# Optimization experiments

Hardware: AMD Instinct MI355X
Metric: run time of the kernel (lower is better)

The kernel has to match this reference:

```python
import jax, jax.numpy as jnp
import numpy as np

N = 200000   # total nodes across batched graphs
E = 3200000  # total edges
G = 1024     # number of graphs
MOL_DIM, HID, OUT = 9, 64, 64


def gcn_conv(x, W, b, src, dst, num_nodes):
    """PyG GCNConv: add self-loops, symmetric deg^{-1/2} normalization, linear first."""
    x = x @ W  # [N, H]
    loop = jnp.arange(num_nodes, dtype=src.dtype)
    s = jnp.concatenate([src, loop])
    d = jnp.concatenate([dst, loop])
    deg = jax.ops.segment_sum(jnp.ones_like(d, dtype=x.dtype), d, num_segments=num_nodes)
    dinv = jnp.where(deg > 0, jax.lax.rsqrt(deg), 0.0)
    norm = dinv[s] * dinv[d]                       # [E+N]
    msgs = x[s] * norm[:, None]                    # gather + scale
    out = jax.ops.segment_sum(msgs, d, num_segments=num_nodes)  # scatter-add
    return out + b


def setup_inputs() -> dict:
    key = jax.random.key(0)
    ks = jax.random.split(key, 12)
    def glorot(k, shp):
        scale = np.sqrt(2.0 / (shp[0] + shp[1])).astype(np.float32)
        return jax.random.normal(k, shp, dtype=jnp.float32) * scale
    return {
        "x": jax.random.normal(ks[0], (N, MOL_DIM), dtype=jnp.float32),
        "edge_index": jax.random.randint(ks[1], (2, E), 0, N, dtype=jnp.int32),
        "edge_attr": jax.random.normal(ks[2], (E, 3), dtype=jnp.float32),
        "batch": jnp.sort(jax.random.randint(ks[3], (N,), 0, G, dtype=jnp.int32)),
        "W1": glorot(ks[4], (MOL_DIM, HID)), "b1": jnp.zeros((HID,), jnp.float32),
        "W2": glorot(ks[5], (HID, HID)),     "b2": jnp.zeros((HID,), jnp.float32),
        "W3": glorot(ks[6], (HID, HID)),     "b3": jnp.zeros((HID,), jnp.float32),
        "Wl": glorot(ks[7], (2 * HID, OUT)), "bl": jnp.zeros((OUT,), jnp.float32),
    }


def reference(x, edge_index, edge_attr, batch, W1, b1, W2, b2, W3, b3, Wl, bl):
    src, dst = edge_index[0], edge_index[1]
    h = jax.nn.relu(gcn_conv(x, W1, b1, src, dst, N))
    h = jax.nn.relu(gcn_conv(h, W2, b2, src, dst, N))
    h = jax.nn.relu(gcn_conv(h, W3, b3, src, dst, N))
    # global mean/max pool over graphs
    counts = jax.ops.segment_sum(jnp.ones((N,), h.dtype), batch, num_segments=G)
    h_sum = jax.ops.segment_sum(h, batch, num_segments=G)
    h_mean = h_sum / jnp.maximum(counts, 1.0)[:, None]
    h_max = jax.ops.segment_max(h, batch, num_segments=G)
    pooled = jnp.concatenate([h_mean, h_max], axis=1)   # [G, 2H]
    return pooled @ Wl + bl
```

## Files before the change

kernel.cpp:

```cpp
#include <hip/hip_runtime.h>

typedef unsigned short u16;
typedef __attribute__((ext_vector_type(8))) short short8;
typedef __attribute__((ext_vector_type(4))) float float4v;

#define HID 64
#define MOLD 9
#define BSH 10
#define NBM 256
#define NBLK 256

__device__ __forceinline__ float bf2f(u16 u) {
    return __uint_as_float(((unsigned)u) << 16);
}
__device__ __forceinline__ u16 f2bf(float f) {
    unsigned x = __float_as_uint(f);
    unsigned r = (x + 0x7FFFu + ((x >> 16) & 1u)) >> 16;
    return (u16)r;
}
__device__ __forceinline__ void unpack_add(uint4 r, float* a) {
    a[0] += __uint_as_float(r.x << 16); a[1] += __uint_as_float(r.x & 0xffff0000u);
    a[2] += __uint_as_float(r.y << 16); a[3] += __uint_as_float(r.y & 0xffff0000u);
    a[4] += __uint_as_float(r.z << 16); a[5] += __uint_as_float(r.z & 0xffff0000u);
    a[6] += __uint_as_float(r.w << 16); a[7] += __uint_as_float(r.w & 0xffff0000u);
}
__device__ __forceinline__ void unpack_set(uint4 r, float* a) {
    a[0] = __uint_as_float(r.x << 16); a[1] = __uint_as_float(r.x & 0xffff0000u);
    a[2] = __uint_as_float(r.y << 16); a[3] = __uint_as_float(r.y & 0xffff0000u);
    a[4] = __uint_as_float(r.z << 16); a[5] = __uint_as_float(r.z & 0xffff0000u);
    a[6] = __uint_as_float(r.w << 16); a[7] = __uint_as_float(r.w & 0xffff0000u);
}

__global__ void k_detect(const u16* __restrict__ p, int n, int* __restrict__ flag) {
    bool bad = false;
    for (int i = threadIdx.x; i < n; i += 256) {
        float v = bf2f(p[i]);
        if (!(v == v) || fabsf(v) > 1000.f) bad = true;
    }
    if (bad) atomicOr(flag, 1);
}

__device__ __forceinline__ void cvt_seg(const void* src, u16* dst, int n, int mode) {
    if (mode) {
        const float* s = (const float*)src;
        for (int i = threadIdx.x; i < n; i += 256) dst[i] = f2bf(s[i]);
    } else {
        const u16* s = (const u16*)src;
        for (int i = threadIdx.x; i < n; i += 256) dst[i] = s[i];
    }
}

__global__ void k_cvt_w(const void* W1, const void* b1, const void* W2, const void* b2,
                        const void* W3, const void* b3, const void* Wl, const void* bl,
                        const int* __restrict__ flag, u16* __restrict__ wbf) {
    int mode = *flag;
    cvt_seg(W1, wbf + 0,     MOLD * HID, mode);
    cvt_seg(b1, wbf + 576,   HID, mode);
    cvt_seg(W2, wbf + 640,   HID * HID, mode);
    cvt_seg(b2, wbf + 4736,  HID, mode);
    cvt_seg(W3, wbf + 4800,  HID * HID, mode);
    cvt_seg(b3, wbf + 8896,  HID, mode);
    cvt_seg(Wl, wbf + 8960,  2 * HID * HID, mode);
    cvt_seg(bl, wbf + 17152, HID, mode);
}

__global__ void k_cvt_x(const void* __restrict__ src, u16* __restrict__ dst, int n,
                        const int* __restrict__ flag) {
    int mode = *flag;
    int i = blockIdx.x * 256 + threadIdx.x;
    if (i >= n) return;
    dst[i] = mode ? f2bf(((const float*)src)[i]) : ((const u16*)src)[i];
}

__global__ __launch_bounds__(256) void k_hist(const int* __restrict__ ei, int E, int nb,
                                              int chunk, int* __restrict__ cntmat) {
    __shared__ int h[NBM];
    int tid = threadIdx.x, k = blockIdx.x;
    for (int i = tid; i < nb; i += 256) h[i] = 0;
    __syncthreads();
    int e0 = k * chunk, e1 = e0 + chunk; if (e1 > E) e1 = E;
    for (int e = e0 + tid; e < e1; e += 256)
        atomicAdd(&h[ei[E + e] >> BSH], 1);
    __syncthreads();
    for (int b = tid; b < nb; b += 256) cntmat[b * NBLK + k] = h[b];
}

__global__ __launch_bounds__(1024) void k_scanmat(int* __restrict__ cntmat, int total) {
    __shared__ int ps[1024];
    int tid = threadIdx.x;
    int chunk = (total + 1023) >> 10;
    int i0 = tid * chunk, i1 = i0 + chunk; if (i1 > total) i1 = total;
    int sum = 0;
    for (int i = i0; i < i1; i++) sum += cntmat[i];
    ps[tid] = sum;
    __syncthreads();
    for (int off = 1; off < 1024; off <<= 1) {
        int t = (tid >= off) ? ps[tid - off] : 0;
        __syncthreads();
        ps[tid] += t;
        __syncthreads();
    }
    int run = ps[tid] - sum;
    for (int i = i0; i < i1; i++) { int c = cntmat[i]; cntmat[i] = run; run += c; }
}

__global__ __launch_bounds__(256) void k_scatter(const int* __restrict__ ei, int E, int nb,
                                                 int chunk, const int* __restrict__ offmat,
                                                 unsigned* __restrict__ staging) {
    __shared__ int cur[NBM];
    int tid = threadIdx.x, k = blockIdx.x;
    for (int b = tid; b < nb; b += 256) cur[b] = offmat[b * NBLK + k];
    __syncthreads();
    int e0 = k * chunk, e1 = e0 + chunk; if (e1 > E) e1 = E;
    for (int e = e0 + tid; e < e1; e += 256) {
        int s = ei[e];
        int d = ei[E + e];
        int b = d >> BSH;
        int p = atomicAdd(&cur[b], 1);
        staging[p] = (unsigned)s | ((unsigned)(d & ((1 << BSH) - 1)) << 18);
    }
}

__global__ __launch_bounds__(256) void k_p4(const unsigned* __restrict__ staging,
                                            const int* __restrict__ offmat, int nb, int N, int E,
                                            int* __restrict__ col, int* __restrict__ rowptr,
                                            float* __restrict__ dinv) {
    __shared__ int cnt[1 << BSH];
    __shared__ int cur[1 << BSH];
    __shared__ int ps[256];
    int b = blockIdx.x, tid = threadIdx.x;
    int s0 = offmat[b * NBLK];
    int s1 = (b == nb - 1) ? E : offmat[(b + 1) * NBLK];
    for (int i = tid; i < (1 << BSH); i += 256) cnt[i] = 0;
    __syncthreads();
    for (int i = s0 + tid; i < s1; i += 256)
        atomicAdd(&cnt[staging[i] >> 18], 1);
    __syncthreads();
    int base4 = tid * 4;
    int c0 = cnt[base4], c1 = cnt[base4 + 1], c2 = cnt[base4 + 2], c3 = cnt[base4 + 3];
    int tsum = c0 + c1 + c2 + c3;
    ps[tid] = tsum;
    __syncthreads();
    for (int off = 1; off < 256; off <<= 1) {
        int t = (tid >= off) ? ps[tid - off] : 0;
        __syncthreads();
        ps[tid] += t;
        __syncthreads();
    }
    int ex = ps[tid] - tsum;
    int o0 = s0 + ex, o1 = o0 + c0, o2 = o1 + c1, o3 = o2 + c2;
    cur[base4] = o0; cur[base4 + 1] = o1; cur[base4 + 2] = o2; cur[base4 + 3] = o3;
    int v = (b << BSH) + base4;
    if (v < N)     { rowptr[v] = o0;     dinv[v] = rsqrtf((float)(c0 + 1)); }
    if (v + 1 < N) { rowptr[v + 1] = o1; dinv[v + 1] = rsqrtf((float)(c1 + 1)); }
    if (v + 2 < N) { rowptr[v + 2] = o2; dinv[v + 2] = rsqrtf((float)(c2 + 1)); }
    if (v + 3 < N) { rowptr[v + 3] = o3; dinv[v + 3] = rsqrtf((float)(c3 + 1)); }
    if (b == nb - 1 && tid == 0) rowptr[N] = E;
    __syncthreads();
    for (int i = s0 + tid; i < s1; i += 256) {
        unsigned w = staging[i];
        int p = atomicAdd(&cur[w >> 18], 1);
        col[p] = (int)(w & 0x3FFFF);
    }
}

__global__ void k_l1(const u16* __restrict__ x, const u16* __restrict__ wseg,
                     const float* __restrict__ dinv, int N, u16* __restrict__ y) {
    __shared__ float w[MOLD * HID];
    int tid = threadIdx.x;
    for (int i = tid; i < MOLD * HID; i += blockDim.x) w[i] = bf2f(wseg[i]);
    __syncthreads();
    int v = blockIdx.x * 4 + (tid >> 6);
    int f = tid & 63;
    if (v >= N) return;
    float acc = 0.f;
#pragma unroll
    for (int k = 0; k < MOLD; k++) acc += bf2f(x[v * MOLD + k]) * w[k * HID + f];
    y[v * HID + f] = f2bf(dinv[v] * acc);
}

__device__ __forceinline__ float gather_node_one(const u16* __restrict__ y,
                                                 const int* __restrict__ rowptr,
                                                 const int* __restrict__ col,
                                                 float dv, float bias,
                                                 int v, int eslot, int fg) {
    float acc[8];
    const u16* yf = y + fg * 8;
    if (eslot == 0) {
        unpack_set(*(const uint4*)(yf + (size_t)v * HID), acc);
    } else {
#pragma unroll
        for (int j = 0; j < 8; j++) acc[j] = 0.f;
    }
    int e = rowptr[v + 1];
    for (int i = rowptr[v] + eslot; i < e; i += 8) {
        int u = col[i];
        uint4 r = *(const uint4*)(yf + (size_t)u * HID);
        unpack_add(r, acc);
    }
    bool e0 = (eslot & 1) != 0, e1 = (eslot & 2) != 0, e2 = (eslot & 4) != 0;
    float s[8];
#pragma unroll
    for (int j = 0; j < 8; j++) s[j] = acc[j] + __shfl_xor(acc[j], 8);
    float b4[4];
#pragma unroll
    for (int k = 0; k < 4; k++) b4[k] = e0 ? s[k + 4] : s[k];
#pragma unroll
    for (int k = 0; k < 4; k++) b4[k] += __shfl_xor(b4[k], 16);
    float c2[2];
    c2[0] = e1 ? b4[2] : b4[0];
    c2[1] = e1 ? b4[3] : b4[1];
    c2[0] += __shfl_xor(c2[0], 32);
    c2[1] += __shfl_xor(c2[1], 32);
    float val = e2 ? c2[1] : c2[0];
    return fmaxf(dv * val + bias, 0.f);
}

__global__ __launch_bounds__(256, 4) void k_agg(
        const u16* __restrict__ y, const int* __restrict__ rowptr,
        const int* __restrict__ col, const float* __restrict__ dinv,
        const u16* __restrict__ bseg, int N, u16* __restrict__ h) {
    int lane = threadIdx.x & 63;
    int eslot = lane >> 3, fg = lane & 7;
    int idx = fg * 8 + ((eslot & 1) << 2) + (eslot & 2) + ((eslot >> 2) & 1);
    float bias = bf2f(bseg[idx]);
    int wid = (blockIdx.x * blockDim.x + threadIdx.x) >> 6;
    int nw = (gridDim.x * blockDim.x) >> 6;
    for (int v = wid; v < N; v += nw) {
        float hv = gather_node_one(y, rowptr, col, dinv[v], bias, v, eslot, fg);
        h[(size_t)v * HID + idx] = f2bf(hv);
    }
}

__global__ __launch_bounds__(256, 4) void k_aggpool(
        const u16* __restrict__ y, const int* __restrict__ rowptr,
        const int* __restrict__ col, const float* __restrict__ dinv,
        const u16* __restrict__ bseg, const int* __restrict__ batch, int N,
        float* __restrict__ hsum, int* __restrict__ hmax, int* __restrict__ cnt) {
    int lane = threadIdx.x & 63;
    int eslot = lane >> 3, fg = lane & 7;
    int idx = fg * 8 + ((eslot & 1) << 2) + (eslot & 2) + ((eslot >> 2) & 1);
    float bias = bf2f(bseg[idx]);
    int wid = (blockIdx.x * blockDim.x + threadIdx.x) >> 6;
    int nw = (gridDim.x * blockDim.x) >> 6;
    int cpw = (N + nw - 1) / nw;
    int v0 = wid * cpw;
    int v1 = v0 + cpw; if (v1 > N) v1 = N;
    int gcur = -1, pcnt = 0;
    float psum = 0.f, pmax = 0.f;
    for (int v = v0; v < v1; ++v) {
        float hv = gather_node_one(y, rowptr, col, dinv[v], bias, v, eslot, fg);
        int g = batch[v];
        if (g != gcur) {
            if (gcur >= 0) {
                atomicAdd(&hsum[gcur * HID + idx], psum);
                atomicMax(&hmax[gcur * HID + idx], __float_as_int(pmax));
                if (lane == 0) atomicAdd(&cnt[gcur], pcnt);
            }
            psum = 0.f; pmax = 0.f; pcnt = 0;
            gcur = g;
        }
        pcnt++;
        psum += hv;
        pmax = fmaxf(pmax, hv);
    }
    if (gcur >= 0) {
        atomicAdd(&hsum[gcur * HID + idx], psum);
        atomicMax(&hmax[gcur * HID + idx], __float_as_int(pmax));
        if (lane == 0) atomicAdd(&cnt[gcur], pcnt);
    }
}

__global__ __launch_bounds__(256, 4) void k_mm(
        const u16* __restrict__ h, const u16* __restrict__ W,
        const float* __restrict__ dinv, int N, u16* __restrict__ y) {
    int lane = threadIdx.x & 63;
    int q = lane >> 4, m = lane & 15;
    int wid = (blockIdx.x * blockDim.x + threadIdx.x) >> 6;
    int nw = (gridDim.x * blockDim.x) >> 6;
    short8 bfrag[4][2];
#pragma unroll
    for (int t = 0; t < 4; ++t)
#pragma unroll
        for (int kh = 0; kh < 2; ++kh) {
            short8 bv;
#pragma unroll
            for (int j = 0; j < 8; ++j)
                bv[j] = (short)W[(kh * 32 + q * 8 + j) * HID + t * 16 + m];
            bfrag[t][kh] = bv;
        }
    const float4v zero = {0.f, 0.f, 0.f, 0.f};
    int ntiles = (N + 15) >> 4;
    for (int tile = wid; tile < ntiles; tile += nw) {
        int base = tile * 16;
        int row = base + m;
        short8 a0 = {0, 0, 0, 0, 0, 0, 0, 0}, a1 = a0;
        if (row < N) {
            uint4 r0 = *(const uint4*)(h + (size_t)row * HID + q * 8);
            uint4 r1 = *(const uint4*)(h + (size_t)row * HID + 32 + q * 8);
            a0 = __builtin_bit_cast(short8, r0);
            a1 = __builtin_bit_cast(short8, r1);
        }
        float4v c[4];
#pragma unroll
        for (int t = 0; t < 4; ++t) c[t] = zero;
#pragma unroll
        for (int t = 0; t < 4; ++t) {
            c[t] = __builtin_amdgcn_mfma_f32_16x16x32_bf16(a0, bfrag[t][0], c[t], 0, 0, 0);
            c[t] = __builtin_amdgcn_mfma_f32_16x16x32_bf16(a1, bfrag[t][1], c[t], 0, 0, 0);
        }
#pragma unroll
        for (int r = 0; r < 4; ++r) {
            int node = base + q * 4 + r;
            if (node < N) {
                float dv = dinv[node];
#pragma unroll
                for (int t = 0; t < 4; ++t)
                    y[(size_t)node * HID + t * 16 + m] = f2bf(c[t][r] * dv);
            }
        }
    }
}

__global__ void k_final(const float* __restrict__ hsum, const int* __restrict__ hmaxi,
                        const int* __restrict__ cnt, const u16* __restrict__ wlseg,
                        const u16* __restrict__ blseg, const int* __restrict__ flag,
                        int G, void* __restrict__ out) {
    __shared__ float w[2 * HID * HID];
    int tid = threadIdx.x;
    for (int i = tid; i < 2 * HID * HID; i += blockDim.x) w[i] = bf2f(wlseg[i]);
    __syncthreads();
    int g = blockIdx.x * 4 + (tid >> 6);
    int f = tid & 63;
    if (g >= G) return;
    float inv = 1.f / fmaxf((float)cnt[g], 1.f);
    float acc = bf2f(blseg[f]);
#pragma unroll 8
    for (int k = 0; k < HID; k++) acc += (hsum[g * HID + k] * inv) * w[k * HID + f];
#pragma unroll 8
    for (int k = 0; k < HID; k++) acc += __int_as_float(hmaxi[g * HID + k]) * w[(HID + k) * HID + f];
    int mode = *flag;
    if (mode) ((float*)out)[g * HID + f] = acc;
    else      ((u16*)out)[g * HID + f] = f2bf(acc);
}

extern "C" void kernel_launch(void* const* d_in, const int* in_sizes, int n_in,
                              void* d_out, int out_size, void* d_ws, size_t ws_size,
                              hipStream_t stream) {
    const void* x  = d_in[0];
    const int*  ei = (const int*)d_in[1];
    const int*  batch = (const int*)d_in[3];

    const int NX = in_sizes[0];
    const int N  = NX / MOLD;
    const int E  = in_sizes[1] / 2;
    const int G  = out_size / HID;
    const int nb = (N + (1 << BSH) - 1) >> BSH;

    char* p = (char*)d_ws;
    auto alloc = [&](size_t bytes) -> char* {
        char* r = p;
        p += (bytes + 255) & ~(size_t)255;
        return r;
    };
    int*   flag    = (int*)alloc(256);
    int*   rowptr  = (int*)alloc((size_t)(N + 1) * 4);
    float* dinv    = (float*)alloc((size_t)N * 4);
    int*   cntmat  = (int*)alloc((size_t)nb * NBLK * 4);
    u16*   wbf     = (u16*)alloc((size_t)17216 * 2);
    int*   colb    = (int*)alloc((size_t)E * 4);
    size_t hb = (size_t)N * HID * 2;
    size_t sb = (size_t)E * 4;
    size_t xb = (size_t)NX * 2;
    size_t ub = hb > sb ? hb : sb; if (xb > ub) ub = xb;
    char* hbuf = alloc(ub);
    unsigned* staging = (unsigned*)hbuf;
    u16*      xbf     = (u16*)hbuf;
    u16*      hbf     = (u16*)hbuf;
    u16*   ybf  = (u16*)alloc((size_t)N * HID * 2);
    float* hsum = (float*)alloc((size_t)G * HID * 4);
    int*   hmax = (int*)alloc((size_t)G * HID * 4);
    int*   cnt  = (int*)alloc((size_t)G * 4);

    hipMemsetAsync(flag, 0, 256, stream);
    hipMemsetAsync(hsum, 0, (size_t)G * HID * 4, stream);
    hipMemsetAsync(hmax, 0, (size_t)G * HID * 4, stream);
    hipMemsetAsync(cnt, 0, (size_t)G * 4, stream);

    k_detect<<<1, 256, 0, stream>>>((const u16*)x, 8192, flag);
    k_cvt_w<<<1, 256, 0, stream>>>(d_in[4], d_in[5], d_in[6], d_in[7],
                                   d_in[8], d_in[9], d_in[10], d_in[11], flag, wbf);

    int chunk = (E + NBLK - 1) / NBLK;
    k_hist<<<NBLK, 256, 0, stream>>>(ei, E, nb, chunk, cntmat);
    k_scanmat<<<1, 1024, 0, stream>>>(cntmat, nb * NBLK);
    k_scatter<<<NBLK, 256, 0, stream>>>(ei, E, nb, chunk, cntmat, staging);
    k_p4<<<nb, 256, 0, stream>>>(staging, cntmat, nb, N, E, colb, rowptr, dinv);

    k_cvt_x<<<(NX + 255) / 256, 256, 0, stream>>>(x, xbf, NX, flag);
    k_l1<<<(N + 3) / 4, 256, 0, stream>>>(xbf, wbf + 0, dinv, N, ybf);

    k_agg<<<2048, 256, 0, stream>>>(ybf, rowptr, colb, dinv, wbf + 576, N, hbf);
    k_mm<<<1024, 256, 0, stream>>>(hbf, wbf + 640, dinv, N, ybf);
    k_agg<<<2048, 256, 0, stream>>>(ybf, rowptr, colb, dinv, wbf + 4736, N, hbf);
    k_mm<<<1024, 256, 0, stream>>>(hbf, wbf + 4800, dinv, N, ybf);
    k_aggpool<<<2048, 256, 0, stream>>>(ybf, rowptr, colb, dinv, wbf + 8896, batch, N,
                                        hsum, hmax, cnt);

    k_final<<<(G + 3) / 4, 256, 0, stream>>>(hsum, hmax, cnt, wbf + 8960, wbf + 17152,
                                             flag, G, d_out);
}
```

Measured before the change: 677.3 us.

## Fuse layer-2 aggregation with layer-3 matmul and inline input conversion

Result: slower. 741.5 us (+9.5%).

```diff
diff --git a/kernel.cpp b/kernel.cpp
--- a/kernel.cpp
+++ b/kernel.cpp
@@ -40,36 +40,23 @@
     if (bad) atomicOr(flag, 1);
 }
 
-__device__ __forceinline__ void cvt_seg(const void* src, u16* dst, int n, int mode) {
-    if (mode) {
-        const float* s = (const float*)src;
-        for (int i = threadIdx.x; i < n; i += 256) dst[i] = f2bf(s[i]);
-    } else {
-        const u16* s = (const u16*)src;
-        for (int i = threadIdx.x; i < n; i += 256) dst[i] = s[i];
-    }
-}
-
 __global__ void k_cvt_w(const void* W1, const void* b1, const void* W2, const void* b2,
                         const void* W3, const void* b3, const void* Wl, const void* bl,
                         const int* __restrict__ flag, u16* __restrict__ wbf) {
     int mode = *flag;
-    cvt_seg(W1, wbf + 0,     MOLD * HID, mode);
-    cvt_seg(b1, wbf + 576,   HID, mode);
-    cvt_seg(W2, wbf + 640,   HID * HID, mode);
-    cvt_seg(b2, wbf + 4736,  HID, mode);
-    cvt_seg(W3, wbf + 4800,  HID * HID, mode);
-    cvt_seg(b3, wbf + 8896,  HID, mode);
-    cvt_seg(Wl, wbf + 8960,  2 * HID * HID, mode);
-    cvt_seg(bl, wbf + 17152, HID, mode);
-}
-
-__global__ void k_cvt_x(const void* __restrict__ src, u16* __restrict__ dst, int n,
-                        const int* __restrict__ flag) {
-    int mode = *flag;
     int i = blockIdx.x * 256 + threadIdx.x;
-    if (i >= n) return;
-    dst[i] = mode ? f2bf(((const float*)src)[i]) : ((const u16*)src)[i];
+    if (i >= 17216) return;
+    const void* s; int base;
+    if (i < 576)        { s = W1; base = 0; }
+    else if (i < 640)   { s = b1; base = 576; }
+    else if (i < 4736)  { s = W2; base = 640; }
+    else if (i < 4800)  { s = b2; base = 4736; }
+    else if (i < 8896)  { s = W3; base = 4800; }
+    else if (i < 8960)  { s = b3; base = 8896; }
+    else if (i < 17152) { s = Wl; base = 8960; }
+    else                { s = bl; base = 17152; }
+    int o = i - base;
+    wbf[i] = mode ? f2bf(((const float*)s)[o]) : ((const u16*)s)[o];
 }
 
 __global__ __launch_bounds__(256) void k_hist(const int* __restrict__ ei, int E, int nb,
@@ -164,10 +151,12 @@
     }
 }
 
-__global__ void k_l1(const u16* __restrict__ x, const u16* __restrict__ wseg,
-                     const float* __restrict__ dinv, int N, u16* __restrict__ y) {
+__global__ void k_l1(const void* __restrict__ x, const u16* __restrict__ wseg,
+                     const float* __restrict__ dinv, const int* __restrict__ flag,
+                     int N, u16* __restrict__ y) {
     __shared__ float w[MOLD * HID];
     int tid = threadIdx.x;
+    int mode = *flag;
     for (int i = tid; i < MOLD * HID; i += blockDim.x) w[i] = bf2f(wseg[i]);
     __syncthreads();
     int v = blockIdx.x * 4 + (tid >> 6);
@@ -175,14 +164,17 @@
     if (v >= N) return;
     float acc = 0.f;
 #pragma unroll
-    for (int k = 0; k < MOLD; k++) acc += bf2f(x[v * MOLD + k]) * w[k * HID + f];
+    for (int k = 0; k < MOLD; k++) {
+        float xv = mode ? ((const float*)x)[v * MOLD + k]
+                        : bf2f(((const u16*)x)[v * MOLD + k]);
+        acc += xv * w[k * HID + f];
+    }
     y[v * HID + f] = f2bf(dinv[v] * acc);
 }
 
-__device__ __forceinline__ float gather_node_one(const u16* __restrict__ y,
+__device__ __forceinline__ float gather_node_raw(const u16* __restrict__ y,
                                                  const int* __restrict__ rowptr,
                                                  const int* __restrict__ col,
-                                                 float dv, float bias,
                                                  int v, int eslot, int fg) {
     float acc[8];
     const u16* yf = y + fg * 8;
@@ -212,8 +204,7 @@
     c2[1] = e1 ? b4[3] : b4[1];
     c2[0] += __shfl_xor(c2[0], 32);
     c2[1] += __shfl_xor(c2[1], 32);
-    float val = e2 ? c2[1] : c2[0];
-    return fmaxf(dv * val + bias, 0.f);
+    return e2 ? c2[1] : c2[0];
 }
 
 __global__ __launch_bounds__(256, 4) void k_agg(
@@ -227,8 +218,68 @@
     int wid = (blockIdx.x * blockDim.x + threadIdx.x) >> 6;
     int nw = (gridDim.x * blockDim.x) >> 6;
     for (int v = wid; v < N; v += nw) {
-        float hv = gather_node_one(y, rowptr, col, dinv[v], bias, v, eslot, fg);
-        h[(size_t)v * HID + idx] = f2bf(hv);
+        float dv = dinv[v];
+        float val = gather_node_raw(y, rowptr, col, v, eslot, fg);
+        float hv = fmaxf(dv * val + bias, 0.f);
+        h[(size_t)v * HID + idx] = f2bf(dv * hv);
+    }
+}
+
+__global__ __launch_bounds__(256, 4) void k_aggmm(
+        const u16* __restrict__ y, const int* __restrict__ rowptr,
+        const int* __restrict__ col, const float* __restrict__ dinv,
+        const u16* __restrict__ W, const u16* __restrict__ bseg,
+        int N, u16* __restrict__ z) {
+    __shared__ u16 wt[HID][72];
+    __shared__ u16 at[4][16][72];
+    int tid = threadIdx.x;
+    for (int i = tid; i < HID * HID; i += 256) {
+        int k = i >> 6, c = i & 63;
+        wt[c][k] = W[i];
+    }
+    __syncthreads();
+    int lane = tid & 63;
+    int wv = tid >> 6;
+    int eslot = lane >> 3, fg = lane & 7;
+    int idx = fg * 8 + ((eslot & 1) << 2) + (eslot & 2) + ((eslot >> 2) & 1);
+    int q = lane >> 4, m = lane & 15;
+    float bb[4];
+#pragma unroll
+    for (int t = 0; t < 4; t++) bb[t] = bf2f(bseg[t * 16 + m]);
+    int gwid = (blockIdx.x * blockDim.x + tid) >> 6;
+    int nw = (gridDim.x * blockDim.x) >> 6;
+    int ngroups = (N + 15) >> 4;
+    for (int g = gwid; g < ngroups; g += nw) {
+        int v0 = g << 4;
+        int vend = N - v0; if (vend > 16) vend = 16;
+        for (int vl = 0; vl < vend; ++vl) {
+            float val = gather_node_raw(y, rowptr, col, v0 + vl, eslot, fg);
+            at[wv][vl][idx] = f2bf(val);
+        }
+        short8 a0 = *(const short8*)&at[wv][m][q * 8];
+        short8 a1 = *(const short8*)&at[wv][m][32 + q * 8];
+        float4v c4[4];
+#pragma unroll
+        for (int t = 0; t < 4; t++) {
+            float4v cz = {0.f, 0.f, 0.f, 0.f};
+            short8 b0 = *(const short8*)&wt[t * 16 + m][q * 8];
+            cz = __builtin_amdgcn_mfma_f32_16x16x32_bf16(a0, b0, cz, 0, 0, 0);
+            short8 b1 = *(const short8*)&wt[t * 16 + m][32 + q * 8];
+            cz = __builtin_amdgcn_mfma_f32_16x16x32_bf16(a1, b1, cz, 0, 0, 0);
+            c4[t] = cz;
+        }
+#pragma unroll
+        for (int r = 0; r < 4; r++) {
+            int node = v0 + q * 4 + r;
+            if (node < N) {
+                float dv = dinv[node];
+#pragma unroll
+                for (int t = 0; t < 4; t++) {
+                    float h = fmaxf(dv * c4[t][r] + bb[t], 0.f);
+                    z[(size_t)node * HID + t * 16 + m] = f2bf(dv * h);
+                }
+            }
+        }
     }
 }
 
@@ -249,7 +300,8 @@
     int gcur = -1, pcnt = 0;
     float psum = 0.f, pmax = 0.f;
     for (int v = v0; v < v1; ++v) {
-        float hv = gather_node_one(y, rowptr, col, dinv[v], bias, v, eslot, fg);
+        float val = gather_node_raw(y, rowptr, col, v, eslot, fg);
+        float hv = fmaxf(dinv[v] * val + bias, 0.f);
         int g = batch[v];
         if (g != gcur) {
             if (gcur >= 0) {
@@ -273,7 +325,7 @@
 
 __global__ __launch_bounds__(256, 4) void k_mm(
         const u16* __restrict__ h, const u16* __restrict__ W,
-        const float* __restrict__ dinv, int N, u16* __restrict__ y) {
+        int N, u16* __restrict__ y) {
     int lane = threadIdx.x & 63;
     int q = lane >> 4, m = lane & 15;
     int wid = (blockIdx.x * blockDim.x + threadIdx.x) >> 6;
@@ -313,10 +365,9 @@
         for (int r = 0; r < 4; ++r) {
             int node = base + q * 4 + r;
             if (node < N) {
-                float dv = dinv[node];
 #pragma unroll
                 for (int t = 0; t < 4; ++t)
-                    y[(size_t)node * HID + t * 16 + m] = f2bf(c[t][r] * dv);
+                    y[(size_t)node * HID + t * 16 + m] = f2bf(c[t][r]);
             }
         }
     }
@@ -371,11 +422,9 @@
     int*   colb    = (int*)alloc((size_t)E * 4);
     size_t hb = (size_t)N * HID * 2;
     size_t sb = (size_t)E * 4;
-    size_t xb = (size_t)NX * 2;
-    size_t ub = hb > sb ? hb : sb; if (xb > ub) ub = xb;
+    size_t ub = hb > sb ? hb : sb;
     char* hbuf = alloc(ub);
     unsigned* staging = (unsigned*)hbuf;
-    u16*      xbf     = (u16*)hbuf;
     u16*      hbf     = (u16*)hbuf;
     u16*   ybf  = (u16*)alloc((size_t)N * HID * 2);
     float* hsum = (float*)alloc((size_t)G * HID * 4);
@@ -388,8 +437,8 @@
     hipMemsetAsync(cnt, 0, (size_t)G * 4, stream);
 
     k_detect<<<1, 256, 0, stream>>>((const u16*)x, 8192, flag);
-    k_cvt_w<<<1, 256, 0, stream>>>(d_in[4], d_in[5], d_in[6], d_in[7],
-                                   d_in[8], d_in[9], d_in[10], d_in[11], flag, wbf);
+    k_cvt_w<<<68, 256, 0, stream>>>(d_in[4], d_in[5], d_in[6], d_in[7],
+                                    d_in[8], d_in[9], d_in[10], d_in[11], flag, wbf);
 
     int chunk = (E + NBLK - 1) / NBLK;
     k_hist<<<NBLK, 256, 0, stream>>>(ei, E, nb, chunk, cntmat);
@@ -397,14 +446,13 @@
     k_scatter<<<NBLK, 256, 0, stream>>>(ei, E, nb, chunk, cntmat, staging);
     k_p4<<<nb, 256, 0, stream>>>(staging, cntmat, nb, N, E, colb, rowptr, dinv);
 
-    k_cvt_x<<<(NX + 255) / 256, 256, 0, stream>>>(x, xbf, NX, flag);
-    k_l1<<<(N + 3) / 4, 256, 0, stream>>>(xbf, wbf + 0, dinv, N, ybf);
+    k_l1<<<(N + 3) / 4, 256, 0, stream>>>(x, wbf + 0, dinv, flag, N, ybf);
 
     k_agg<<<2048, 256, 0, stream>>>(ybf, rowptr, colb, dinv, wbf + 576, N, hbf);
-    k_mm<<<1024, 256, 0, stream>>>(hbf, wbf + 640, dinv, N, ybf);
-    k_agg<<<2048, 256, 0, stream>>>(ybf, rowptr, colb, dinv, wbf + 4736, N, hbf);
-    k_mm<<<1024, 256, 0, stream>>>(hbf, wbf + 4800, dinv, N, ybf);
-    k_aggpool<<<2048, 256, 0, stream>>>(ybf, rowptr, colb, dinv, wbf + 8896, batch, N,
+    k_aggmm<<<2048, 256, 0, stream>>>(hbf, rowptr, colb, dinv, wbf + 640, wbf + 4736,
+                                      N, ybf);
+    k_mm<<<1024, 256, 0, stream>>>(ybf, wbf + 4800, N, hbf);
+    k_aggpool<<<2048, 256, 0, stream>>>(hbf, rowptr, colb, dinv, wbf + 8896, batch, N,
                                         hsum, hmax, cnt);
 
     k_final<<<(G + 3) / 4, 256, 0, stream>>>(hsum, hmax, cnt, wbf + 8960, wbf + 17152,
```

## Aggregate raw 9-dim features before layer-1 matmul and parallelize weight conversion

Applied to the files above, without the earlier changes.

Measured after the change: 592.1 us. -12.6%, faster.

```diff
diff --git a/kernel.cpp b/kernel.cpp
--- a/kernel.cpp
+++ b/kernel.cpp
@@ -30,6 +30,10 @@
     a[4] = __uint_as_float(r.z << 16); a[5] = __uint_as_float(r.z & 0xffff0000u);
     a[6] = __uint_as_float(r.w << 16); a[7] = __uint_as_float(r.w & 0xffff0000u);
 }
+__device__ __forceinline__ void unpack_add2(uint2 r, float* a) {
+    a[0] += __uint_as_float(r.x << 16); a[1] += __uint_as_float(r.x & 0xffff0000u);
+    a[2] += __uint_as_float(r.y << 16); a[3] += __uint_as_float(r.y & 0xffff0000u);
+}
 
 __global__ void k_detect(const u16* __restrict__ p, int n, int* __restrict__ flag) {
     bool bad = false;
@@ -40,36 +44,23 @@
     if (bad) atomicOr(flag, 1);
 }
 
-__device__ __forceinline__ void cvt_seg(const void* src, u16* dst, int n, int mode) {
-    if (mode) {
-        const float* s = (const float*)src;
-        for (int i = threadIdx.x; i < n; i += 256) dst[i] = f2bf(s[i]);
-    } else {
-        const u16* s = (const u16*)src;
-        for (int i = threadIdx.x; i < n; i += 256) dst[i] = s[i];
-    }
-}
-
 __global__ void k_cvt_w(const void* W1, const void* b1, const void* W2, const void* b2,
                         const void* W3, const void* b3, const void* Wl, const void* bl,
                         const int* __restrict__ flag, u16* __restrict__ wbf) {
     int mode = *flag;
-    cvt_seg(W1, wbf + 0,     MOLD * HID, mode);
-    cvt_seg(b1, wbf + 576,   HID, mode);
-    cvt_seg(W2, wbf + 640,   HID * HID, mode);
-    cvt_seg(b2, wbf + 4736,  HID, mode);
-    cvt_seg(W3, wbf + 4800,  HID * HID, mode);
-    cvt_seg(b3, wbf + 8896,  HID, mode);
-    cvt_seg(Wl, wbf + 8960,  2 * HID * HID, mode);
-    cvt_seg(bl, wbf + 17152, HID, mode);
-}
-
-__global__ void k_cvt_x(const void* __restrict__ src, u16* __restrict__ dst, int n,
-                        const int* __restrict__ flag) {
-    int mode = *flag;
     int i = blockIdx.x * 256 + threadIdx.x;
-    if (i >= n) return;
-    dst[i] = mode ? f2bf(((const float*)src)[i]) : ((const u16*)src)[i];
+    if (i >= 17216) return;
+    const void* s; int base;
+    if (i < 576)        { s = W1; base = 0; }
+    else if (i < 640)   { s = b1; base = 576; }
+    else if (i < 4736)  { s = W2; base = 640; }
+    else if (i < 4800)  { s = b2; base = 4736; }
+    else if (i < 8896)  { s = W3; base = 4800; }
+    else if (i < 8960)  { s = b3; base = 8896; }
+    else if (i < 17152) { s = Wl; base = 8960; }
+    else                { s = bl; base = 17152; }
+    int o = i - base;
+    wbf[i] = mode ? f2bf(((const float*)s)[o]) : ((const u16*)s)[o];
 }
 
 __global__ __launch_bounds__(256) void k_hist(const int* __restrict__ ei, int E, int nb,
@@ -164,19 +155,71 @@
     }
 }
 
-__global__ void k_l1(const u16* __restrict__ x, const u16* __restrict__ wseg,
-                     const float* __restrict__ dinv, int N, u16* __restrict__ y) {
-    __shared__ float w[MOLD * HID];
-    int tid = threadIdx.x;
-    for (int i = tid; i < MOLD * HID; i += blockDim.x) w[i] = bf2f(wseg[i]);
-    __syncthreads();
-    int v = blockIdx.x * 4 + (tid >> 6);
-    int f = tid & 63;
-    if (v >= N) return;
-    float acc = 0.f;
-#pragma unroll
-    for (int k = 0; k < MOLD; k++) acc += bf2f(x[v * MOLD + k]) * w[k * HID + f];
-    y[v * HID + f] = f2bf(dinv[v] * acc);
+__global__ void k_cvt_x(const void* __restrict__ x, const float* __restrict__ dinv,
+                        const int* __restrict__ flag, int N, u16* __restrict__ xd) {
+    int mode = *flag;
+    int i = blockIdx.x * 256 + threadIdx.x;
+    if (i >= N * 16) return;
+    int v = i >> 4, f = i & 15;
+    float val = 0.f;
+    if (f < MOLD) {
+        val = mode ? ((const float*)x)[v * MOLD + f]
+                   : bf2f(((const u16*)x)[v * MOLD + f]);
+        val *= dinv[v];
+    }
+    xd[i] = f2bf(val);
+}
+
+__global__ __launch_bounds__(256, 4) void k_aggx(
+        const u16* __restrict__ xd, const int* __restrict__ rowptr,
+        const int* __restrict__ col, const float* __restrict__ dinv,
+        const u16* __restrict__ W1, const u16* __restrict__ b1,
+        int N, u16* __restrict__ h1) {
+    int lane = threadIdx.x & 63;
+    int eslot = lane >> 2, fq = lane & 3;
+    float w1r[MOLD];
+#pragma unroll
+    for (int k = 0; k < MOLD; k++) w1r[k] = bf2f(W1[k * HID + lane]);
+    float bias = bf2f(b1[lane]);
+    bool sel0 = ((lane >> 2) & 1) != 0, sel1 = ((lane >> 3) & 1) != 0;
+    int wid = (blockIdx.x * blockDim.x + threadIdx.x) >> 6;
+    int nw = (gridDim.x * blockDim.x) >> 6;
+    for (int v = wid; v < N; v += nw) {
+        float acc[4];
+        if (eslot == 0) {
+            uint2 r = *(const uint2*)(xd + (size_t)v * 16 + fq * 4);
+            acc[0] = __uint_as_float(r.x << 16); acc[1] = __uint_as_float(r.x & 0xffff0000u);
+            acc[2] = __uint_as_float(r.y << 16); acc[3] = __uint_as_float(r.y & 0xffff0000u);
+        } else {
+#pragma unroll
+            for (int j = 0; j < 4; j++) acc[j] = 0.f;
+        }
+        int e = rowptr[v + 1];
+        for (int i = rowptr[v] + eslot; i < e; i += 16) {
+            int u = col[i];
+            uint2 r = *(const uint2*)(xd + (size_t)u * 16 + fq * 4);
+            unpack_add2(r, acc);
+        }
+        float s0 = acc[0] + __shfl_xor(acc[0], 4);
+        float s1 = acc[1] + __shfl_xor(acc[1], 4);
+        float s2 = acc[2] + __shfl_xor(acc[2], 4);
+        float s3 = acc[3] + __shfl_xor(acc[3], 4);
+        float t0 = sel0 ? s2 : s0;
+        float t1 = sel0 ? s3 : s1;
+        t0 += __shfl_xor(t0, 8);
+        t1 += __shfl_xor(t1, 8);
+        float val = sel1 ? t1 : t0;
+        val += __shfl_xor(val, 16);
+        val += __shfl_xor(val, 32);
+        float accf = 0.f;
+#pragma unroll
+        for (int k = 0; k < MOLD; k++) {
+            int Lk = (k >> 2) | ((k & 2) << 1) | ((k & 1) << 3);
+            accf += __shfl(val, Lk) * w1r[k];
+        }
+        float h = fmaxf(dinv[v] * accf + bias, 0.f);
+        h1[(size_t)v * HID + lane] = f2bf(h);
+    }
 }
 
 __device__ __forceinline__ float gather_node_one(const u16* __restrict__ y,
@@ -371,11 +414,11 @@
     int*   colb    = (int*)alloc((size_t)E * 4);
     size_t hb = (size_t)N * HID * 2;
     size_t sb = (size_t)E * 4;
-    size_t xb = (size_t)NX * 2;
-    size_t ub = hb > sb ? hb : sb; if (xb > ub) ub = xb;
+    size_t xs = (size_t)N * 16 * 2;
+    size_t ub = hb; if (sb > ub) ub = sb; if (xs > ub) ub = xs;
     char* hbuf = alloc(ub);
     unsigned* staging = (unsigned*)hbuf;
-    u16*      xbf     = (u16*)hbuf;
+    u16*      xd      = (u16*)hbuf;
     u16*      hbf     = (u16*)hbuf;
     u16*   ybf  = (u16*)alloc((size_t)N * HID * 2);
     float* hsum = (float*)alloc((size_t)G * HID * 4);
@@ -388,8 +431,8 @@
     hipMemsetAsync(cnt, 0, (size_t)G * 4, stream);
 
     k_detect<<<1, 256, 0, stream>>>((const u16*)x, 8192, flag);
-    k_cvt_w<<<1, 256, 0, stream>>>(d_in[4], d_in[5], d_in[6], d_in[7],
-                                   d_in[8], d_in[9], d_in[10], d_in[11], flag, wbf);
+    k_cvt_w<<<68, 256, 0, stream>>>(d_in[4], d_in[5], d_in[6], d_in[7],
+                                    d_in[8], d_in[9], d_in[10], d_in[11], flag, wbf);
 
     int chunk = (E + NBLK - 1) / NBLK;
     k_hist<<<NBLK, 256, 0, stream>>>(ei, E, nb, chunk, cntmat);
@@ -397,14 +440,13 @@
     k_scatter<<<NBLK, 256, 0, stream>>>(ei, E, nb, chunk, cntmat, staging);
     k_p4<<<nb, 256, 0, stream>>>(staging, cntmat, nb, N, E, colb, rowptr, dinv);
 
-    k_cvt_x<<<(NX + 255) / 256, 256, 0, stream>>>(x, xbf, NX, flag);
-    k_l1<<<(N + 3) / 4, 256, 0, stream>>>(xbf, wbf + 0, dinv, N, ybf);
-
-    k_agg<<<2048, 256, 0, stream>>>(ybf, rowptr, colb, dinv, wbf + 576, N, hbf);
-    k_mm<<<1024, 256, 0, stream>>>(hbf, wbf + 640, dinv, N, ybf);
-    k_agg<<<2048, 256, 0, stream>>>(ybf, rowptr, colb, dinv, wbf + 4736, N, hbf);
-    k_mm<<<1024, 256, 0, stream>>>(hbf, wbf + 4800, dinv, N, ybf);
-    k_aggpool<<<2048, 256, 0, stream>>>(ybf, rowptr, colb, dinv, wbf + 8896, batch, N,
+    k_cvt_x<<<(N * 16 + 255) / 256, 256, 0, stream>>>(x, dinv, flag, N, xd);
+    k_aggx<<<2048, 256, 0, stream>>>(xd, rowptr, colb, dinv, wbf + 0, wbf + 576,
+                                     N, ybf);
+    k_mm<<<1024, 256, 0, stream>>>(ybf, wbf + 640, dinv, N, hbf);
+    k_agg<<<2048, 256, 0, stream>>>(hbf, rowptr, colb, dinv, wbf + 4736, N, ybf);
+    k_mm<<<1024, 256, 0, stream>>>(ybf, wbf + 4800, dinv, N, hbf);
+    k_aggpool<<<2048, 256, 0, stream>>>(hbf, rowptr, colb, dinv, wbf + 8896, batch, N,
                                         hsum, hmax, cnt);
 
     k_final<<<(G + 3) / 4, 256, 0, stream>>>(hsum, hmax, cnt, wbf + 8960, wbf + 17152,
```
